# Performance work log

Measured on AMD Instinct MI355X. Metric: run time of the kernel, lower is better.

The kernel has to match this reference:

```python
import jax, jax.numpy as jnp
import numpy as np

DIM = 32
N_ENTITY = 500000
N_RELATION = 64
N_USER = 100000
N_ITEM = 200000
B = 4096
K = 64
L = 2


def setup_inputs() -> dict:
    key = jax.random.key(0)
    ks = jax.random.split(key, 14)
    users = jax.random.randint(ks[0], (B,), 0, N_USER)
    items = jax.random.randint(ks[1], (B,), 0, N_ITEM)
    hop0_items = jax.random.randint(ks[2], (B, K), 0, N_ENTITY)
    heads = jax.random.randint(ks[3], (L, B, K), 0, N_ENTITY)
    relations = jax.random.randint(ks[4], (L, B, K), 0, N_RELATION)
    tails = jax.random.randint(ks[5], (L, B, K), 0, N_ENTITY)
    # xavier-uniform-style embedding tables
    def xavier(k, shape):
        bound = float(np.sqrt(6.0 / (shape[0] + shape[1])))
        return jax.random.uniform(k, shape, jnp.float32, -bound, bound)
    entity_emb = xavier(ks[6], (N_ENTITY, DIM))
    relation_emb = xavier(ks[7], (N_RELATION, DIM))
    rec_user_emb = xavier(ks[8], (N_USER, DIM))
    rec_item_emb = xavier(ks[9], (N_ITEM, DIM))
    # RNN params (torch default init: U(-1/sqrt(hidden), 1/sqrt(hidden)))
    b = 1.0 / float(np.sqrt(DIM))
    W_ih = jax.random.uniform(ks[10], (DIM, 2 * DIM), jnp.float32, -b, b)
    W_hh = jax.random.uniform(ks[11], (DIM, DIM), jnp.float32, -b, b)
    b_ih = jax.random.uniform(ks[12], (DIM,), jnp.float32, -b, b)
    b_hh = jax.random.uniform(ks[13], (DIM,), jnp.float32, -b, b)
    return {
        "users": users, "items": items, "hop0_items": hop0_items,
        "heads": heads, "relations": relations, "tails": tails,
        "entity_emb": entity_emb, "relation_emb": relation_emb,
        "rec_user_emb": rec_user_emb, "rec_item_emb": rec_item_emb,
        "W_ih": W_ih, "W_hh": W_hh, "b_ih": b_ih, "b_hh": b_hh,
    }


def reference(users, items, hop0_items, heads, relations, tails,
              entity_emb, relation_emb, rec_user_emb, rec_item_emb,
              W_ih, W_hh, b_ih, b_hh):
    # hop-0: sum of item embeddings in each user's seed set  [B, dim]
    o = entity_emb[hop0_items].sum(axis=1)
    n_hops = heads.shape[0]
    for l in range(n_hops):
        h = entity_emb[heads[l]]        # [B, K, d]
        r = relation_emb[relations[l]]  # [B, K, d]
        tl = entity_emb[tails[l]]       # [B, K, d]
        hr = jnp.concatenate([h, r], axis=-1)   # [B, K, 2d]
        tr = jnp.concatenate([tl, r], axis=-1)  # [B, K, 2d]
        # attention over the K triples of each user
        pi = jax.nn.softmax((hr * tr).sum(axis=-1), axis=1)[..., None]  # [B,K,1]
        # 2-step tanh RNN over sequence (hr, tr), h0 = 0; take final hidden state
        h1 = jnp.tanh(jnp.einsum('bke,de->bkd', hr, W_ih) + b_ih + b_hh)
        h2 = jnp.tanh(jnp.einsum('bke,de->bkd', tr, W_ih)
                      + jnp.einsum('bkd,ed->bke', h1, W_hh) + b_ih + b_hh)
        o = o + (pi * h2).sum(axis=1)
    user_embeddings = o + rec_user_emb[users]
    item_embeddings = entity_emb[items] + rec_item_emb[items]
    return jax.nn.sigmoid((user_embeddings * item_embeddings).sum(axis=1))
```

## Files before the change

### kernel.cpp

```cpp
#include <hip/hip_runtime.h>

#define DIM 32
#define KK 64
#define WPB 4
#define WIH_STRIDE 144
#define WHH_STRIDE 80
#define REL_STRIDE 80
#define LDS_WIH (32 * WIH_STRIDE)
#define LDS_WHH (32 * WHH_STRIDE)
#define LDS_REL (64 * REL_STRIDE)

typedef short bf16x8 __attribute__((ext_vector_type(8)));
typedef float f32x16 __attribute__((ext_vector_type(16)));
typedef unsigned int u32x4 __attribute__((ext_vector_type(4)));

__device__ __forceinline__ float rcp_fast(float x) { return __builtin_amdgcn_rcpf(x); }

__device__ __forceinline__ float tanh_fast(float x) {
    float t = __expf(2.0f * x);
    return 1.0f - 2.0f * rcp_fast(t + 1.0f);
}

__device__ __forceinline__ unsigned pk2(float lo, float hi) {
    return __builtin_amdgcn_perm(__builtin_bit_cast(unsigned, hi),
                                 __builtin_bit_cast(unsigned, lo), 0x07060302u);
}

__device__ __forceinline__ bf16x8 pack8(float4 a, float4 b) {
    u32x4 u;
    u[0] = pk2(a.x, a.y); u[1] = pk2(a.z, a.w);
    u[2] = pk2(b.x, b.y); u[3] = pk2(b.z, b.w);
    return __builtin_bit_cast(bf16x8, u);
}

__device__ __forceinline__ float dot4(float4 a, float4 b) {
    float s = a.x * b.x;
    s = fmaf(a.y, b.y, s); s = fmaf(a.z, b.z, s); s = fmaf(a.w, b.w, s);
    return s;
}

__global__ __launch_bounds__(256, 3) void ripple_k1(
    const int* __restrict__ users,
    const int* __restrict__ items,
    const int* __restrict__ hop0_items,
    const int* __restrict__ heads,
    const int* __restrict__ relations,
    const int* __restrict__ tails,
    const float* __restrict__ entity_emb,
    const float* __restrict__ relation_emb,
    const float* __restrict__ rec_user_emb,
    const float* __restrict__ rec_item_emb,
    const float* __restrict__ W_ih,
    const float* __restrict__ W_hh,
    const float* __restrict__ b_ih,
    const float* __restrict__ b_hh,
    float* __restrict__ ws,
    const int B)
{
    __shared__ __align__(16) unsigned char lds[LDS_WIH + LDS_WHH + LDS_REL + 256];
    unsigned char* wihL = lds;
    unsigned char* whhL = lds + LDS_WIH;
    unsigned char* relL = lds + LDS_WIH + LDS_WHH;
    float* rrL = (float*)(lds + LDS_WIH + LDS_WHH + LDS_REL);

    const int tid = threadIdx.x;

    #pragma unroll
    for (int c = 0; c < 4; ++c) {
        int i = tid + 256 * c;
        int row = i >> 5, dw = i & 31;
        *(unsigned*)(wihL + row * WIH_STRIDE + dw * 4) =
            pk2(W_ih[row * 64 + 2 * dw], W_ih[row * 64 + 2 * dw + 1]);
    }
    #pragma unroll
    for (int c = 0; c < 2; ++c) {
        int i = tid + 256 * c;
        int row = i >> 4, dw = i & 15;
        *(unsigned*)(whhL + row * WHH_STRIDE + dw * 4) =
            pk2(W_hh[row * 32 + 2 * dw], W_hh[row * 32 + 2 * dw + 1]);
    }
    #pragma unroll
    for (int c = 0; c < 4; ++c) {
        int i = tid + 256 * c;
        int row = i >> 4, dw = i & 15;
        *(unsigned*)(relL + row * REL_STRIDE + dw * 4) =
            pk2(relation_emb[row * 32 + 2 * dw], relation_emb[row * 32 + 2 * dw + 1]);
    }
    if (tid < 64) {
        float s = 0.0f;
        #pragma unroll
        for (int e = 0; e < DIM; ++e) {
            float v = relation_emb[tid * DIM + e];
            s = fmaf(v, v, s);
        }
        rrL[tid] = s;
    }
    __syncthreads();

    const int wv   = tid >> 6;
    const int lane = tid & 63;
    const int h5   = lane >> 5;
    const int p    = lane & 31;
    const int w    = blockIdx.x * WPB + wv;
    if (w >= 3 * B) return;

    int role, b0;
    if (w < B)          { role = 0; b0 = w; }
    else if (w < 2 * B) { role = 1; b0 = w - B; }
    else                { role = 2; b0 = w - 2 * B; }
    const int b = __builtin_amdgcn_readfirstlane(b0);

    if (role == 0) {
        const int it = __builtin_amdgcn_readfirstlane(items[b]);
        const int uu = __builtin_amdgcn_readfirstlane(users[b]);
        const int iA = hop0_items[b * KK + p];
        const int iB = hop0_items[b * KK + 32 + p];
        const float* a0 = entity_emb + (size_t)iA * DIM + 8 * h5;
        const float* b0p = entity_emb + (size_t)iB * DIM + 8 * h5;
        float4 vA0 = *(const float4*)(a0);
        float4 vA1 = *(const float4*)(a0 + 4);
        float4 vA2 = *(const float4*)(a0 + 16);
        float4 vA3 = *(const float4*)(a0 + 20);
        float4 vB0 = *(const float4*)(b0p);
        float4 vB1 = *(const float4*)(b0p + 4);
        float4 vB2 = *(const float4*)(b0p + 16);
        float4 vB3 = *(const float4*)(b0p + 20);

        float q[DIM];
        #pragma unroll
        for (int d = 0; d < DIM; ++d)
            q[d] = entity_emb[(size_t)it * DIM + d] + rec_item_emb[(size_t)it * DIM + d];
        float up = 0.0f;
        #pragma unroll
        for (int d = 0; d < DIM; ++d)
            up = fmaf(rec_user_emb[(size_t)uu * DIM + d], q[d], up);

        float4 c0a, c0b, c1a, c1b;
        {
            float tmp[16];
            #pragma unroll
            for (int e = 0; e < 8; ++e) {
                tmp[e]     = h5 ? q[8 + e]  : q[e];
                tmp[8 + e] = h5 ? q[24 + e] : q[16 + e];
            }
            c0a = make_float4(tmp[0], tmp[1], tmp[2], tmp[3]);
            c0b = make_float4(tmp[4], tmp[5], tmp[6], tmp[7]);
            c1a = make_float4(tmp[8], tmp[9], tmp[10], tmp[11]);
            c1b = make_float4(tmp[12], tmp[13], tmp[14], tmp[15]);
        }
        float part = dot4(vA0, c0a) + dot4(vA1, c0b) + dot4(vA2, c1a) + dot4(vA3, c1b)
                   + dot4(vB0, c0a) + dot4(vB1, c0b) + dot4(vB2, c1a) + dot4(vB3, c1b);
        #pragma unroll
        for (int m = 1; m <= 32; m <<= 1) part += __shfl_xor(part, m, 64);
        if (lane == 0) ws[b] = part + up;
        return;
    }

    const int l = role - 1;
    const int base = (l * B + b) * KK;

    const int iAh = heads[base + p],       iBh = heads[base + 32 + p];
    const int iAr = relations[base + p],   iBr = relations[base + 32 + p];
    const int iAt = tails[base + p],       iBt = tails[base + 32 + p];

    float4 gh[8], gt[8];
    {
        const float* a = entity_emb + (size_t)iAh * DIM + 8 * h5;
        const float* c = entity_emb + (size_t)iBh * DIM + 8 * h5;
        gh[0] = *(const float4*)(a);      gh[1] = *(const float4*)(a + 4);
        gh[2] = *(const float4*)(a + 16); gh[3] = *(const float4*)(a + 20);
        gh[4] = *(const float4*)(c);      gh[5] = *(const float4*)(c + 4);
        gh[6] = *(const float4*)(c + 16); gh[7] = *(const float4*)(c + 20);
    }
    {
        const float* a = entity_emb + (size_t)iAt * DIM + 8 * h5;
        const float* c = entity_emb + (size_t)iBt * DIM + 8 * h5;
        gt[0] = *(const float4*)(a);      gt[1] = *(const float4*)(a + 4);
        gt[2] = *(const float4*)(a + 16); gt[3] = *(const float4*)(a + 20);
        gt[4] = *(const float4*)(c);      gt[5] = *(const float4*)(c + 4);
        gt[6] = *(const float4*)(c + 16); gt[7] = *(const float4*)(c + 20);
    }

    bf16x8 rf[2][2];
    #pragma unroll
    for (int kt = 0; kt < 2; ++kt) {
        rf[0][kt] = __builtin_bit_cast(bf16x8,
            *(const u32x4*)(relL + iAr * REL_STRIDE + kt * 32 + h5 * 16));
        rf[1][kt] = __builtin_bit_cast(bf16x8,
            *(const u32x4*)(relL + iBr * REL_STRIDE + kt * 32 + h5 * 16));
    }
    const float rrA = rrL[iAr];
    const float rrB = rrL[iBr];

    const int it = __builtin_amdgcn_readfirstlane(items[b]);
    float qu[DIM], bu[DIM];
    #pragma unroll
    for (int d = 0; d < DIM; ++d) {
        qu[d] = entity_emb[(size_t)it * DIM + d] + rec_item_emb[(size_t)it * DIM + d];
        bu[d] = b_ih[d] + b_hh[d];
    }
    float qf[16], bv[16];
    #pragma unroll
    for (int Q = 0; Q < 4; ++Q)
        #pragma unroll
        for (int j = 0; j < 4; ++j) {
            qf[4*Q+j] = h5 ? qu[8*Q + 4 + j] : qu[8*Q + j];
            bv[4*Q+j] = h5 ? bu[8*Q + 4 + j] : bu[8*Q + j];
        }

    float scA = 0.0f, scB = 0.0f;
    #pragma unroll
    for (int i = 0; i < 4; ++i) scA += dot4(gh[i], gt[i]);
    #pragma unroll
    for (int i = 4; i < 8; ++i) scB += dot4(gh[i], gt[i]);

    bf16x8 hf[2][2], tf[2][2];
    #pragma unroll
    for (int nt = 0; nt < 2; ++nt)
        #pragma unroll
        for (int kt = 0; kt < 2; ++kt) {
            hf[nt][kt] = pack8(gh[nt*4 + kt*2], gh[nt*4 + kt*2 + 1]);
            tf[nt][kt] = pack8(gt[nt*4 + kt*2], gt[nt*4 + kt*2 + 1]);
        }

    bf16x8 wihF[4], whhF[2];
    #pragma unroll
    for (int kt = 0; kt < 4; ++kt)
        wihF[kt] = __builtin_bit_cast(bf16x8,
            *(const u32x4*)(wihL + p * WIH_STRIDE + kt * 32 + h5 * 16));
    #pragma unroll
    for (int kt = 0; kt < 2; ++kt)
        whhF[kt] = __builtin_bit_cast(bf16x8,
            *(const u32x4*)(whhL + p * WHH_STRIDE + kt * 32 + h5 * 16));

    f32x16 accA[2], accB[2];
    {
        f32x16 bias_v;
        #pragma unroll
        for (int j = 0; j < 16; ++j) bias_v[j] = bv[j];
        accA[0] = bias_v; accA[1] = bias_v;
    }
    #pragma unroll
    for (int nt = 0; nt < 2; ++nt)
        #pragma unroll
        for (int kt = 0; kt < 2; ++kt)
            accA[nt] = __builtin_amdgcn_mfma_f32_32x32x16_bf16(
                wihF[2 + kt], rf[nt][kt], accA[nt], 0, 0, 0);
    accB[0] = accA[0]; accB[1] = accA[1];
    #pragma unroll
    for (int nt = 0; nt < 2; ++nt)
        #pragma unroll
        for (int kt = 0; kt < 2; ++kt)
            accB[nt] = __builtin_amdgcn_mfma_f32_32x32x16_bf16(
                wihF[kt], hf[nt][kt], accB[nt], 0, 0, 0);
    #pragma unroll
    for (int nt = 0; nt < 2; ++nt)
        #pragma unroll
        for (int kt = 0; kt < 2; ++kt)
            accA[nt] = __builtin_amdgcn_mfma_f32_32x32x16_bf16(
                wihF[kt], tf[nt][kt], accA[nt], 0, 0, 0);

    unsigned dwA[2][4], dwB[2][4];
    #pragma unroll
    for (int nt = 0; nt < 2; ++nt)
        #pragma unroll
        for (int Q = 0; Q < 4; ++Q) {
            dwA[nt][Q] = pk2(tanh_fast(accB[nt][4*Q+0]), tanh_fast(accB[nt][4*Q+1]));
            dwB[nt][Q] = pk2(tanh_fast(accB[nt][4*Q+2]), tanh_fast(accB[nt][4*Q+3]));
        }
    #pragma unroll
    for (int nt = 0; nt < 2; ++nt)
        #pragma unroll
        for (int kt = 0; kt < 2; ++kt) {
            const unsigned ownA = h5 ? dwA[nt][2*kt+1] : dwA[nt][2*kt];
            const unsigned ownB = h5 ? dwB[nt][2*kt+1] : dwB[nt][2*kt];
            const unsigned sndA = h5 ? dwA[nt][2*kt]   : dwA[nt][2*kt+1];
            const unsigned sndB = h5 ? dwB[nt][2*kt]   : dwB[nt][2*kt+1];
            const unsigned rcvA = __shfl_xor(sndA, 32, 64);
            const unsigned rcvB = __shfl_xor(sndB, 32, 64);
            u32x4 u;
            u[0] = h5 ? rcvA : ownA;
            u[1] = h5 ? rcvB : ownB;
            u[2] = h5 ? ownA : rcvA;
            u[3] = h5 ? ownB : rcvB;
            accA[nt] = __builtin_amdgcn_mfma_f32_32x32x16_bf16(
                whhF[kt], __builtin_bit_cast(bf16x8, u), accA[nt], 0, 0, 0);
        }

    scA += __shfl_xor(scA, 32, 64);
    scB += __shfl_xor(scB, 32, 64);
    const float e0 = __expf(scA + rrA);
    const float e1 = __expf(scB + rrB);

    float sd0 = 0.0f, sd1 = 0.0f;
    #pragma unroll
    for (int j = 0; j < 16; ++j) sd0 = fmaf(tanh_fast(accA[0][j]), qf[j], sd0);
    #pragma unroll
    for (int j = 0; j < 16; ++j) sd1 = fmaf(tanh_fast(accA[1][j]), qf[j], sd1);
    sd0 += __shfl_xor(sd0, 32, 64);
    sd1 += __shfl_xor(sd1, 32, 64);

    float num = e0 * sd0 + e1 * sd1;
    float den = e0 + e1;
    #pragma unroll
    for (int m = 1; m <= 16; m <<= 1) {
        num += __shfl_xor(num, m, 64);
        den += __shfl_xor(den, m, 64);
    }
    if (lane == 0) ws[(1 + l) * B + b] = num * rcp_fast(den);
}

__global__ __launch_bounds__(256) void ripple_k2(
    const float* __restrict__ ws, float* __restrict__ out, const int B)
{
    const int i = blockIdx.x * 256 + threadIdx.x;
    if (i < B) {
        const float s = ws[i] + ws[B + i] + ws[2 * B + i];
        out[i] = rcp_fast(1.0f + __expf(-s));
    }
}

extern "C" void kernel_launch(void* const* d_in, const int* in_sizes, int n_in,
                              void* d_out, int out_size, void* d_ws, size_t ws_size,
                              hipStream_t stream)
{
    const int* users = (const int*)d_in[0];
    const int* items = (const int*)d_in[1];
    const int* hop0  = (const int*)d_in[2];
    const int* heads = (const int*)d_in[3];
    const int* rels  = (const int*)d_in[4];
    const int* tails = (const int*)d_in[5];
    const float* entity_emb   = (const float*)d_in[6];
    const float* relation_emb = (const float*)d_in[7];
    const float* rec_user_emb = (const float*)d_in[8];
    const float* rec_item_emb = (const float*)d_in[9];
    const float* W_ih = (const float*)d_in[10];
    const float* W_hh = (const float*)d_in[11];
    const float* b_ih = (const float*)d_in[12];
    const float* b_hh = (const float*)d_in[13];
    float* out = (float*)d_out;
    float* ws  = (float*)d_ws;

    const int B = in_sizes[0];
    const int blocks1 = (3 * B + WPB - 1) / WPB;
    hipLaunchKernelGGL(ripple_k1, dim3(blocks1), dim3(256), 0, stream,
                       users, items, hop0, heads, rels, tails,
                       entity_emb, relation_emb, rec_user_emb, rec_item_emb,
                       W_ih, W_hh, b_ih, b_hh, ws, B);
    const int blocks2 = (B + 255) / 256;
    hipLaunchKernelGGL(ripple_k2, dim3(blocks2), dim3(256), 0, stream,
                       ws, out, B);
}
```

Before: 50.73 us.

## Fuse hop roles into one wave per user and gather from bf16 entity copy

Merges the three per-role waves (hop0 and two hops) into a single wave per batch row, computing the final sigmoid in-kernel and dropping the second reduction kernel. Adds a pre-pass that converts the whole 500k x 32 entity table to bf16 in workspace, so gathers move half the bytes. The conversion streams the full 64 MB table every call, which likely costs far more than the gathered rows it saves (about 1.3M rows). Attention scores now use bf16-rounded inputs, which loses some precision.

```diff
diff --git a/kernel.cpp b/kernel.cpp
--- a/kernel.cpp
+++ b/kernel.cpp
@@ -26,6 +26,9 @@
                                  __builtin_bit_cast(unsigned, lo), 0x07060302u);
 }
 
+__device__ __forceinline__ float lo16(unsigned u) { return __builtin_bit_cast(float, u << 16); }
+__device__ __forceinline__ float hi16(unsigned u) { return __builtin_bit_cast(float, u & 0xffff0000u); }
+
 __device__ __forceinline__ bf16x8 pack8(float4 a, float4 b) {
     u32x4 u;
     u[0] = pk2(a.x, a.y); u[1] = pk2(a.z, a.w);
@@ -39,7 +42,23 @@
     return s;
 }
 
-__global__ __launch_bounds__(256, 3) void ripple_k1(
+__global__ __launch_bounds__(256) void cvt_bf16(
+    const float* __restrict__ in, unsigned* __restrict__ outp, const long n8)
+{
+    long i = (long)blockIdx.x * 256 + threadIdx.x;
+    const long stride = (long)gridDim.x * 256;
+    for (; i < n8; i += stride) {
+        const float4 a = ((const float4*)in)[2 * i];
+        const float4 c = ((const float4*)in)[2 * i + 1];
+        u32x4 u;
+        u[0] = pk2(a.x, a.y); u[1] = pk2(a.z, a.w);
+        u[2] = pk2(c.x, c.y); u[3] = pk2(c.z, c.w);
+        ((u32x4*)outp)[i] = u;
+    }
+}
+
+template <bool BF16>
+__global__ __launch_bounds__(256, 2) void ripple_fused(
     const int* __restrict__ users,
     const int* __restrict__ items,
     const int* __restrict__ hop0_items,
@@ -54,7 +73,8 @@
     const float* __restrict__ W_hh,
     const float* __restrict__ b_ih,
     const float* __restrict__ b_hh,
-    float* __restrict__ ws,
+    const unsigned* __restrict__ tabbf,
+    float* __restrict__ out,
     const int B)
 {
     __shared__ __align__(16) unsigned char lds[LDS_WIH + LDS_WHH + LDS_REL + 256];
@@ -101,104 +121,59 @@
     const int lane = tid & 63;
     const int h5   = lane >> 5;
     const int p    = lane & 31;
-    const int w    = blockIdx.x * WPB + wv;
-    if (w >= 3 * B) return;
-
-    int role, b0;
-    if (w < B)          { role = 0; b0 = w; }
-    else if (w < 2 * B) { role = 1; b0 = w - B; }
-    else                { role = 2; b0 = w - 2 * B; }
-    const int b = __builtin_amdgcn_readfirstlane(b0);
-
-    if (role == 0) {
-        const int it = __builtin_amdgcn_readfirstlane(items[b]);
-        const int uu = __builtin_amdgcn_readfirstlane(users[b]);
-        const int iA = hop0_items[b * KK + p];
-        const int iB = hop0_items[b * KK + 32 + p];
-        const float* a0 = entity_emb + (size_t)iA * DIM + 8 * h5;
-        const float* b0p = entity_emb + (size_t)iB * DIM + 8 * h5;
-        float4 vA0 = *(const float4*)(a0);
-        float4 vA1 = *(const float4*)(a0 + 4);
-        float4 vA2 = *(const float4*)(a0 + 16);
-        float4 vA3 = *(const float4*)(a0 + 20);
-        float4 vB0 = *(const float4*)(b0p);
-        float4 vB1 = *(const float4*)(b0p + 4);
-        float4 vB2 = *(const float4*)(b0p + 16);
-        float4 vB3 = *(const float4*)(b0p + 20);
-
-        float q[DIM];
-        #pragma unroll
-        for (int d = 0; d < DIM; ++d)
-            q[d] = entity_emb[(size_t)it * DIM + d] + rec_item_emb[(size_t)it * DIM + d];
-        float up = 0.0f;
-        #pragma unroll
-        for (int d = 0; d < DIM; ++d)
-            up = fmaf(rec_user_emb[(size_t)uu * DIM + d], q[d], up);
-
-        float4 c0a, c0b, c1a, c1b;
-        {
-            float tmp[16];
-            #pragma unroll
-            for (int e = 0; e < 8; ++e) {
-                tmp[e]     = h5 ? q[8 + e]  : q[e];
-                tmp[8 + e] = h5 ? q[24 + e] : q[16 + e];
-            }
-            c0a = make_float4(tmp[0], tmp[1], tmp[2], tmp[3]);
-            c0b = make_float4(tmp[4], tmp[5], tmp[6], tmp[7]);
-            c1a = make_float4(tmp[8], tmp[9], tmp[10], tmp[11]);
-            c1b = make_float4(tmp[12], tmp[13], tmp[14], tmp[15]);
-        }
-        float part = dot4(vA0, c0a) + dot4(vA1, c0b) + dot4(vA2, c1a) + dot4(vA3, c1b)
-                   + dot4(vB0, c0a) + dot4(vB1, c0b) + dot4(vB2, c1a) + dot4(vB3, c1b);
-        #pragma unroll
-        for (int m = 1; m <= 32; m <<= 1) part += __shfl_xor(part, m, 64);
-        if (lane == 0) ws[b] = part + up;
-        return;
-    }
-
-    const int l = role - 1;
-    const int base = (l * B + b) * KK;
-
-    const int iAh = heads[base + p],       iBh = heads[base + 32 + p];
-    const int iAr = relations[base + p],   iBr = relations[base + 32 + p];
-    const int iAt = tails[base + p],       iBt = tails[base + 32 + p];
-
-    float4 gh[8], gt[8];
-    {
-        const float* a = entity_emb + (size_t)iAh * DIM + 8 * h5;
-        const float* c = entity_emb + (size_t)iBh * DIM + 8 * h5;
-        gh[0] = *(const float4*)(a);      gh[1] = *(const float4*)(a + 4);
-        gh[2] = *(const float4*)(a + 16); gh[3] = *(const float4*)(a + 20);
-        gh[4] = *(const float4*)(c);      gh[5] = *(const float4*)(c + 4);
-        gh[6] = *(const float4*)(c + 16); gh[7] = *(const float4*)(c + 20);
-    }
-    {
-        const float* a = entity_emb + (size_t)iAt * DIM + 8 * h5;
-        const float* c = entity_emb + (size_t)iBt * DIM + 8 * h5;
-        gt[0] = *(const float4*)(a);      gt[1] = *(const float4*)(a + 4);
-        gt[2] = *(const float4*)(a + 16); gt[3] = *(const float4*)(a + 20);
-        gt[4] = *(const float4*)(c);      gt[5] = *(const float4*)(c + 4);
-        gt[6] = *(const float4*)(c + 16); gt[7] = *(const float4*)(c + 20);
-    }
-
-    bf16x8 rf[2][2];
-    #pragma unroll
-    for (int kt = 0; kt < 2; ++kt) {
-        rf[0][kt] = __builtin_bit_cast(bf16x8,
-            *(const u32x4*)(relL + iAr * REL_STRIDE + kt * 32 + h5 * 16));
-        rf[1][kt] = __builtin_bit_cast(bf16x8,
-            *(const u32x4*)(relL + iBr * REL_STRIDE + kt * 32 + h5 * 16));
-    }
-    const float rrA = rrL[iAr];
-    const float rrB = rrL[iBr];
+    const int bb_  = blockIdx.x * WPB + wv;
+    if (bb_ >= B) return;
+    const int b = __builtin_amdgcn_readfirstlane(bb_);
+
+    const int i0A = hop0_items[b * KK + p];
+    const int i0B = hop0_items[b * KK + 32 + p];
+    int ihA[2], ihB[2], irA[2], irB[2], itA[2], itB[2];
+    #pragma unroll
+    for (int l = 0; l < 2; ++l) {
+        const int base = (l * B + b) * KK;
+        ihA[l] = heads[base + p];     ihB[l] = heads[base + 32 + p];
+        irA[l] = relations[base + p]; irB[l] = relations[base + 32 + p];
+        itA[l] = tails[base + p];     itB[l] = tails[base + 32 + p];
+    }
+
+    u32x4 g0[2][2], gH[2][2][2], gT[2][2][2];
+    if constexpr (BF16) {
+        const u32x4* T4 = (const u32x4*)tabbf;
+        #pragma unroll
+        for (int kt = 0; kt < 2; ++kt) {
+            g0[0][kt] = T4[(size_t)i0A * 4 + 2 * kt + h5];
+            g0[1][kt] = T4[(size_t)i0B * 4 + 2 * kt + h5];
+        }
+        #pragma unroll
+        for (int l = 0; l < 2; ++l)
+            #pragma unroll
+            for (int kt = 0; kt < 2; ++kt) {
+                gH[l][0][kt] = T4[(size_t)ihA[l] * 4 + 2 * kt + h5];
+                gH[l][1][kt] = T4[(size_t)ihB[l] * 4 + 2 * kt + h5];
+                gT[l][0][kt] = T4[(size_t)itA[l] * 4 + 2 * kt + h5];
+                gT[l][1][kt] = T4[(size_t)itB[l] * 4 + 2 * kt + h5];
+            }
+    }
 
     const int it = __builtin_amdgcn_readfirstlane(items[b]);
+    const int uu = __builtin_amdgcn_readfirstlane(users[b]);
     float qu[DIM], bu[DIM];
     #pragma unroll
     for (int d = 0; d < DIM; ++d) {
         qu[d] = entity_emb[(size_t)it * DIM + d] + rec_item_emb[(size_t)it * DIM + d];
         bu[d] = b_ih[d] + b_hh[d];
     }
+    float up = 0.0f;
+    #pragma unroll
+    for (int d = 0; d < DIM; ++d)
+        up = fmaf(rec_user_emb[(size_t)uu * DIM + d], qu[d], up);
+
+    float qfa[8], qfb[8];
+    #pragma unroll
+    for (int j = 0; j < 8; ++j) {
+        qfa[j] = h5 ? qu[8 + j]  : qu[j];
+        qfb[j] = h5 ? qu[24 + j] : qu[16 + j];
+    }
     float qf[16], bv[16];
     #pragma unroll
     for (int Q = 0; Q < 4; ++Q)
@@ -208,20 +183,35 @@
             bv[4*Q+j] = h5 ? bu[8*Q + 4 + j] : bu[8*Q + j];
         }
 
-    float scA = 0.0f, scB = 0.0f;
-    #pragma unroll
-    for (int i = 0; i < 4; ++i) scA += dot4(gh[i], gt[i]);
-    #pragma unroll
-    for (int i = 4; i < 8; ++i) scB += dot4(gh[i], gt[i]);
-
-    bf16x8 hf[2][2], tf[2][2];
-    #pragma unroll
-    for (int nt = 0; nt < 2; ++nt)
-        #pragma unroll
-        for (int kt = 0; kt < 2; ++kt) {
-            hf[nt][kt] = pack8(gh[nt*4 + kt*2], gh[nt*4 + kt*2 + 1]);
-            tf[nt][kt] = pack8(gt[nt*4 + kt*2], gt[nt*4 + kt*2 + 1]);
-        }
+    float part = 0.0f;
+    if constexpr (BF16) {
+        #pragma unroll
+        for (int nt = 0; nt < 2; ++nt)
+            #pragma unroll
+            for (int j = 0; j < 4; ++j) {
+                part = fmaf(lo16(g0[nt][0][j]), qfa[2*j],     part);
+                part = fmaf(hi16(g0[nt][0][j]), qfa[2*j + 1], part);
+                part = fmaf(lo16(g0[nt][1][j]), qfb[2*j],     part);
+                part = fmaf(hi16(g0[nt][1][j]), qfb[2*j + 1], part);
+            }
+    } else {
+        const float* a0  = entity_emb + (size_t)i0A * DIM + 8 * h5;
+        const float* b0p = entity_emb + (size_t)i0B * DIM + 8 * h5;
+        float4 vA0 = *(const float4*)(a0);      float4 vA1 = *(const float4*)(a0 + 4);
+        float4 vA2 = *(const float4*)(a0 + 16); float4 vA3 = *(const float4*)(a0 + 20);
+        float4 vB0 = *(const float4*)(b0p);      float4 vB1 = *(const float4*)(b0p + 4);
+        float4 vB2 = *(const float4*)(b0p + 16); float4 vB3 = *(const float4*)(b0p + 20);
+        float4 c0a = make_float4(qfa[0], qfa[1], qfa[2], qfa[3]);
+        float4 c0b = make_float4(qfa[4], qfa[5], qfa[6], qfa[7]);
+        float4 c1a = make_float4(qfb[0], qfb[1], qfb[2], qfb[3]);
+        float4 c1b = make_float4(qfb[4], qfb[5], qfb[6], qfb[7]);
+        part = dot4(vA0, c0a) + dot4(vA1, c0b) + dot4(vA2, c1a) + dot4(vA3, c1b)
+             + dot4(vB0, c0a) + dot4(vB1, c0b) + dot4(vB2, c1a) + dot4(vB3, c1b);
+    }
+    #pragma unroll
+    for (int m = 1; m <= 32; m <<= 1) part += __shfl_xor(part, m, 64);
+
+    float tot = part + up;
 
     bf16x8 wihF[4], whhF[2];
     #pragma unroll
@@ -233,91 +223,147 @@
         whhF[kt] = __builtin_bit_cast(bf16x8,
             *(const u32x4*)(whhL + p * WHH_STRIDE + kt * 32 + h5 * 16));
 
-    f32x16 accA[2], accB[2];
-    {
-        f32x16 bias_v;
-        #pragma unroll
-        for (int j = 0; j < 16; ++j) bias_v[j] = bv[j];
-        accA[0] = bias_v; accA[1] = bias_v;
-    }
-    #pragma unroll
-    for (int nt = 0; nt < 2; ++nt)
-        #pragma unroll
-        for (int kt = 0; kt < 2; ++kt)
-            accA[nt] = __builtin_amdgcn_mfma_f32_32x32x16_bf16(
-                wihF[2 + kt], rf[nt][kt], accA[nt], 0, 0, 0);
-    accB[0] = accA[0]; accB[1] = accA[1];
-    #pragma unroll
-    for (int nt = 0; nt < 2; ++nt)
-        #pragma unroll
-        for (int kt = 0; kt < 2; ++kt)
-            accB[nt] = __builtin_amdgcn_mfma_f32_32x32x16_bf16(
-                wihF[kt], hf[nt][kt], accB[nt], 0, 0, 0);
-    #pragma unroll
-    for (int nt = 0; nt < 2; ++nt)
-        #pragma unroll
-        for (int kt = 0; kt < 2; ++kt)
-            accA[nt] = __builtin_amdgcn_mfma_f32_32x32x16_bf16(
-                wihF[kt], tf[nt][kt], accA[nt], 0, 0, 0);
-
-    unsigned dwA[2][4], dwB[2][4];
-    #pragma unroll
-    for (int nt = 0; nt < 2; ++nt)
-        #pragma unroll
-        for (int Q = 0; Q < 4; ++Q) {
-            dwA[nt][Q] = pk2(tanh_fast(accB[nt][4*Q+0]), tanh_fast(accB[nt][4*Q+1]));
-            dwB[nt][Q] = pk2(tanh_fast(accB[nt][4*Q+2]), tanh_fast(accB[nt][4*Q+3]));
-        }
-    #pragma unroll
-    for (int nt = 0; nt < 2; ++nt)
+    #pragma unroll
+    for (int l = 0; l < 2; ++l) {
+        bf16x8 hfr[2][2], tfr[2][2];
+        float scA = 0.0f, scB = 0.0f;
+        if constexpr (BF16) {
+            #pragma unroll
+            for (int kt = 0; kt < 2; ++kt)
+                #pragma unroll
+                for (int j = 0; j < 4; ++j) {
+                    scA = fmaf(lo16(gH[l][0][kt][j]), lo16(gT[l][0][kt][j]), scA);
+                    scA = fmaf(hi16(gH[l][0][kt][j]), hi16(gT[l][0][kt][j]), scA);
+                    scB = fmaf(lo16(gH[l][1][kt][j]), lo16(gT[l][1][kt][j]), scB);
+                    scB = fmaf(hi16(gH[l][1][kt][j]), hi16(gT[l][1][kt][j]), scB);
+                }
+            #pragma unroll
+            for (int nt = 0; nt < 2; ++nt)
+                #pragma unroll
+                for (int kt = 0; kt < 2; ++kt) {
+                    hfr[nt][kt] = __builtin_bit_cast(bf16x8, gH[l][nt][kt]);
+                    tfr[nt][kt] = __builtin_bit_cast(bf16x8, gT[l][nt][kt]);
+                }
+        } else {
+            float4 fh[8], ft[8];
+            {
+                const float* a = entity_emb + (size_t)ihA[l] * DIM + 8 * h5;
+                const float* c = entity_emb + (size_t)ihB[l] * DIM + 8 * h5;
+                fh[0] = *(const float4*)(a);      fh[1] = *(const float4*)(a + 4);
+                fh[2] = *(const float4*)(a + 16); fh[3] = *(const float4*)(a + 20);
+                fh[4] = *(const float4*)(c);      fh[5] = *(const float4*)(c + 4);
+                fh[6] = *(const float4*)(c + 16); fh[7] = *(const float4*)(c + 20);
+            }
+            {
+                const float* a = entity_emb + (size_t)itA[l] * DIM + 8 * h5;
+                const float* c = entity_emb + (size_t)itB[l] * DIM + 8 * h5;
+                ft[0] = *(const float4*)(a);      ft[1] = *(const float4*)(a + 4);
+                ft[2] = *(const float4*)(a + 16); ft[3] = *(const float4*)(a + 20);
+                ft[4] = *(const float4*)(c);      ft[5] = *(const float4*)(c + 4);
+                ft[6] = *(const float4*)(c + 16); ft[7] = *(const float4*)(c + 20);
+            }
+            #pragma unroll
+            for (int i = 0; i < 4; ++i) scA += dot4(fh[i], ft[i]);
+            #pragma unroll
+            for (int i = 4; i < 8; ++i) scB += dot4(fh[i], ft[i]);
+            #pragma unroll
+            for (int nt = 0; nt < 2; ++nt)
+                #pragma unroll
+                for (int kt = 0; kt < 2; ++kt) {
+                    hfr[nt][kt] = pack8(fh[nt*4 + kt*2], fh[nt*4 + kt*2 + 1]);
+                    tfr[nt][kt] = pack8(ft[nt*4 + kt*2], ft[nt*4 + kt*2 + 1]);
+                }
+        }
+
+        bf16x8 rfr[2][2];
         #pragma unroll
         for (int kt = 0; kt < 2; ++kt) {
-            const unsigned ownA = h5 ? dwA[nt][2*kt+1] : dwA[nt][2*kt];
-            const unsigned ownB = h5 ? dwB[nt][2*kt+1] : dwB[nt][2*kt];
-            const unsigned sndA = h5 ? dwA[nt][2*kt]   : dwA[nt][2*kt+1];
-            const unsigned sndB = h5 ? dwB[nt][2*kt]   : dwB[nt][2*kt+1];
-            const unsigned rcvA = __shfl_xor(sndA, 32, 64);
-            const unsigned rcvB = __shfl_xor(sndB, 32, 64);
-            u32x4 u;
-            u[0] = h5 ? rcvA : ownA;
-            u[1] = h5 ? rcvB : ownB;
-            u[2] = h5 ? ownA : rcvA;
-            u[3] = h5 ? ownB : rcvB;
-            accA[nt] = __builtin_amdgcn_mfma_f32_32x32x16_bf16(
-                whhF[kt], __builtin_bit_cast(bf16x8, u), accA[nt], 0, 0, 0);
-        }
-
-    scA += __shfl_xor(scA, 32, 64);
-    scB += __shfl_xor(scB, 32, 64);
-    const float e0 = __expf(scA + rrA);
-    const float e1 = __expf(scB + rrB);
-
-    float sd0 = 0.0f, sd1 = 0.0f;
-    #pragma unroll
-    for (int j = 0; j < 16; ++j) sd0 = fmaf(tanh_fast(accA[0][j]), qf[j], sd0);
-    #pragma unroll
-    for (int j = 0; j < 16; ++j) sd1 = fmaf(tanh_fast(accA[1][j]), qf[j], sd1);
-    sd0 += __shfl_xor(sd0, 32, 64);
-    sd1 += __shfl_xor(sd1, 32, 64);
-
-    float num = e0 * sd0 + e1 * sd1;
-    float den = e0 + e1;
-    #pragma unroll
-    for (int m = 1; m <= 16; m <<= 1) {
-        num += __shfl_xor(num, m, 64);
-        den += __shfl_xor(den, m, 64);
-    }
-    if (lane == 0) ws[(1 + l) * B + b] = num * rcp_fast(den);
-}
-
-__global__ __launch_bounds__(256) void ripple_k2(
-    const float* __restrict__ ws, float* __restrict__ out, const int B)
-{
-    const int i = blockIdx.x * 256 + threadIdx.x;
-    if (i < B) {
-        const float s = ws[i] + ws[B + i] + ws[2 * B + i];
-        out[i] = rcp_fast(1.0f + __expf(-s));
-    }
+            rfr[0][kt] = __builtin_bit_cast(bf16x8,
+                *(const u32x4*)(relL + irA[l] * REL_STRIDE + kt * 32 + h5 * 16));
+            rfr[1][kt] = __builtin_bit_cast(bf16x8,
+                *(const u32x4*)(relL + irB[l] * REL_STRIDE + kt * 32 + h5 * 16));
+        }
+        const float rrA = rrL[irA[l]];
+        const float rrB = rrL[irB[l]];
+
+        f32x16 accA[2], accB[2];
+        {
+            f32x16 bias_v;
+            #pragma unroll
+            for (int j = 0; j < 16; ++j) bias_v[j] = bv[j];
+            accA[0] = bias_v; accA[1] = bias_v;
+        }
+        #pragma unroll
+        for (int nt = 0; nt < 2; ++nt)
+            #pragma unroll
+            for (int kt = 0; kt < 2; ++kt)
+                accA[nt] = __builtin_amdgcn_mfma_f32_32x32x16_bf16(
+                    wihF[2 + kt], rfr[nt][kt], accA[nt], 0, 0, 0);
+        accB[0] = accA[0]; accB[1] = accA[1];
+        #pragma unroll
+        for (int nt = 0; nt < 2; ++nt)
+            #pragma unroll
+            for (int kt = 0; kt < 2; ++kt)
+                accB[nt] = __builtin_amdgcn_mfma_f32_32x32x16_bf16(
+                    wihF[kt], hfr[nt][kt], accB[nt], 0, 0, 0);
+        #pragma unroll
+        for (int nt = 0; nt < 2; ++nt)
+            #pragma unroll
+            for (int kt = 0; kt < 2; ++kt)
+                accA[nt] = __builtin_amdgcn_mfma_f32_32x32x16_bf16(
+                    wihF[kt], tfr[nt][kt], accA[nt], 0, 0, 0);
+
+        unsigned dwA[2][4], dwB[2][4];
+        #pragma unroll
+        for (int nt = 0; nt < 2; ++nt)
+            #pragma unroll
+            for (int Q = 0; Q < 4; ++Q) {
+                dwA[nt][Q] = pk2(tanh_fast(accB[nt][4*Q+0]), tanh_fast(accB[nt][4*Q+1]));
+                dwB[nt][Q] = pk2(tanh_fast(accB[nt][4*Q+2]), tanh_fast(accB[nt][4*Q+3]));
+            }
+        #pragma unroll
+        for (int nt = 0; nt < 2; ++nt)
+            #pragma unroll
+            for (int kt = 0; kt < 2; ++kt) {
+                const unsigned ownA = h5 ? dwA[nt][2*kt+1] : dwA[nt][2*kt];
+                const unsigned ownB = h5 ? dwB[nt][2*kt+1] : dwB[nt][2*kt];
+                const unsigned sndA = h5 ? dwA[nt][2*kt]   : dwA[nt][2*kt+1];
+                const unsigned sndB = h5 ? dwB[nt][2*kt]   : dwB[nt][2*kt+1];
+                const unsigned rcvA = __shfl_xor(sndA, 32, 64);
+                const unsigned rcvB = __shfl_xor(sndB, 32, 64);
+                u32x4 u;
+                u[0] = h5 ? rcvA : ownA;
+                u[1] = h5 ? rcvB : ownB;
+                u[2] = h5 ? ownA : rcvA;
+                u[3] = h5 ? ownB : rcvB;
+                accA[nt] = __builtin_amdgcn_mfma_f32_32x32x16_bf16(
+                    whhF[kt], __builtin_bit_cast(bf16x8, u), accA[nt], 0, 0, 0);
+            }
+
+        float sA = scA + __shfl_xor(scA, 32, 64);
+        float sB = scB + __shfl_xor(scB, 32, 64);
+        const float e0 = __expf(sA + rrA);
+        const float e1 = __expf(sB + rrB);
+
+        float sd0 = 0.0f, sd1 = 0.0f;
+        #pragma unroll
+        for (int j = 0; j < 16; ++j) sd0 = fmaf(tanh_fast(accA[0][j]), qf[j], sd0);
+        #pragma unroll
+        for (int j = 0; j < 16; ++j) sd1 = fmaf(tanh_fast(accA[1][j]), qf[j], sd1);
+        sd0 += __shfl_xor(sd0, 32, 64);
+        sd1 += __shfl_xor(sd1, 32, 64);
+
+        float num = e0 * sd0 + e1 * sd1;
+        float den = e0 + e1;
+        #pragma unroll
+        for (int m = 1; m <= 16; m <<= 1) {
+            num += __shfl_xor(num, m, 64);
+            den += __shfl_xor(den, m, 64);
+        }
+        tot += num * rcp_fast(den);
+    }
+
+    if (lane == 0) out[b] = rcp_fast(1.0f + __expf(-tot));
 }
 
 extern "C" void kernel_launch(void* const* d_in, const int* in_sizes, int n_in,
@@ -339,15 +385,25 @@
     const float* b_ih = (const float*)d_in[12];
     const float* b_hh = (const float*)d_in[13];
     float* out = (float*)d_out;
-    float* ws  = (float*)d_ws;
 
     const int B = in_sizes[0];
-    const int blocks1 = (3 * B + WPB - 1) / WPB;
-    hipLaunchKernelGGL(ripple_k1, dim3(blocks1), dim3(256), 0, stream,
-                       users, items, hop0, heads, rels, tails,
-                       entity_emb, relation_emb, rec_user_emb, rec_item_emb,
-                       W_ih, W_hh, b_ih, b_hh, ws, B);
-    const int blocks2 = (B + 255) / 256;
-    hipLaunchKernelGGL(ripple_k2, dim3(blocks2), dim3(256), 0, stream,
-                       ws, out, B);
-}
+    const long nent_elems = (long)in_sizes[6];
+    const size_t need = (size_t)nent_elems * 2;
+    const int blocks1 = (B + WPB - 1) / WPB;
+
+    if (ws_size >= need) {
+        hipLaunchKernelGGL(cvt_bf16, dim3(2048), dim3(256), 0, stream,
+                           entity_emb, (unsigned*)d_ws, nent_elems / 8);
+        hipLaunchKernelGGL((ripple_fused<true>), dim3(blocks1), dim3(256), 0, stream,
+                           users, items, hop0, heads, rels, tails,
+                           entity_emb, relation_emb, rec_user_emb, rec_item_emb,
+                           W_ih, W_hh, b_ih, b_hh,
+                           (const unsigned*)d_ws, out, B);
+    } else {
+        hipLaunchKernelGGL((ripple_fused<false>), dim3(blocks1), dim3(256), 0, stream,
+                           users, items, hop0, heads, rels, tails,
+                           entity_emb, relation_emb, rec_user_emb, rec_item_emb,
+                           W_ih, W_hh, b_ih, b_hh,
+                           (const unsigned*)nullptr, out, B);
+    }
+}
```

New measurement: 57.54 us. 1.13x slower.
